# Kernel tuning notes

Hardware: AMD Instinct MI355X
Metric: run time of the kernel (lower is better)

Reference implementation:

```python
import jax, jax.numpy as jnp
import numpy as np

B, N, C, T = 16, 96, 4, 256
H, DT, DP, P, TOUT = 128, 16, 128, 4, 64
DIN = H + DT
LEAK = 0.1


def setup_inputs():
    key = jax.random.key(0)
    ks = jax.random.split(key, 16)
    rn = lambda k, shp, s: jax.random.normal(k, shp, dtype=jnp.float32) * s
    return {
        'X_in': jax.random.normal(ks[0], (B, N, C, T), dtype=jnp.float32),
        'phases': jax.random.randint(ks[1], (B,), 0, P),
        'gru_Wih': rn(ks[2], (N, 3 * H, C), 0.1),
        'gru_Whh': rn(ks[3], (N, 3 * H, H), 0.08),
        'gru_bih': jnp.zeros((N, 3 * H), jnp.float32),
        'gru_bhh': jnp.zeros((N, 3 * H), jnp.float32),
        'ln_g': jnp.ones((H,), jnp.float32),
        'ln_b': jnp.zeros((H,), jnp.float32),
        'tpos_w': rn(ks[4], (DT, 1), 0.5),
        'tpos_b': jnp.zeros((DT,), jnp.float32),
        'S': rn(ks[5], (P, N, N), 0.1),
        'G': rn(ks[6], (P, N), 0.1),
        'W_self': rn(ks[7], (DP, DIN), 0.05),
        'W_neigh': rn(ks[8], (DP, DIN), 0.05),
        'sn_u': jax.random.normal(ks[9], (DP,), dtype=jnp.float32),
        'k_w': rn(ks[10], (DP, DP), 0.05),
        'v_w': rn(ks[11], (DP, DP), 0.05),
        'cell_Wih': rn(ks[12], (3 * DP, DP + C), 0.05),
        'cell_Whh': rn(ks[13], (3 * DP, DP), 0.05),
        'cell_bih': jnp.zeros((3 * DP,), jnp.float32),
        'cell_bhh': jnp.zeros((3 * DP,), jnp.float32),
        'read_w': rn(ks[14], (C, DP), 0.05),
        'read_b': jnp.zeros((C,), jnp.float32),
        'log_tau': jnp.asarray(np.log(1.0 / np.sqrt(DP)), dtype=jnp.float32),
    }


def _encode(X, Wih, Whh, bih, bhh, g, b):
    # Per-region GRU (distinct weights per node), torch gate order r,z,n.
    xs = jnp.moveaxis(X, -1, 0)  # [T,B,N,C]
    h0 = jnp.zeros((B, N, H), X.dtype)
    def step(h, xt):
        gi = jnp.einsum('bnc,ngc->bng', xt, Wih) + bih
        gh = jnp.einsum('bnh,ngh->bng', h, Whh) + bhh
        ir, iz, inn = jnp.split(gi, 3, axis=-1)
        hr, hz, hn = jnp.split(gh, 3, axis=-1)
        r = jax.nn.sigmoid(ir + hr)
        z = jax.nn.sigmoid(iz + hz)
        n = jnp.tanh(inn + r * hn)
        hnew = (1.0 - z) * n + z * h
        return hnew, hnew
    _, ys = jax.lax.scan(step, h0, xs)  # [T,B,N,H]
    mu = ys.mean(-1, keepdims=True)
    var = ys.var(-1, keepdims=True)
    ys = (ys - mu) * jax.lax.rsqrt(var + 1e-5) * g + b
    return jnp.moveaxis(ys, 0, 2)  # [B,N,T,H]


def _phase_adj(S, G, phases):
    I = jnp.eye(N, dtype=S.dtype)
    S0 = S * (1.0 - I)
    denom = jnp.clip(jnp.abs(S0).sum(-1, keepdims=True), 1e-6, None)
    An = S0 / denom
    gg = jax.nn.softplus(G) + 1e-6
    gg = gg * (N / jnp.clip(gg.sum(-1, keepdims=True), 1e-6, None))
    return An[phases] * gg[phases][..., None]  # [B,N,N]


def _spectral_normalize(W, u):
    v = W.T @ u
    v = v / (jnp.linalg.norm(v) + 1e-12)
    u2 = W @ v
    u2 = u2 / (jnp.linalg.norm(u2) + 1e-12)
    u2 = jax.lax.stop_gradient(u2)
    v = jax.lax.stop_gradient(v)
    sigma = u2 @ (W @ v)
    return W / sigma


def _head(Z, A, k_w, v_w, cWih, cWhh, cbih, cbhh, rw, rb, log_tau):
    BN = B * N
    M = Z.reshape(BN, T, DP)
    K = M @ k_w.T
    V = M @ v_w.T
    h0 = M[:, -1, :]
    y0 = jnp.zeros((BN, C), Z.dtype)
    scale = jnp.exp(log_tau)
    def step(carry, _):
        h, y = carry
        yb = y.reshape(B, N, C)
        yb = yb + 0.3 * jnp.einsum('bij,bjc->bic', A, yb)
        y = yb.reshape(BN, C)
        scores = jnp.einsum('mtd,md->mt', K, h) * scale
        alpha = jax.nn.softmax(scores, axis=-1)
        ctx = jnp.einsum('mt,mtd->md', alpha, V)
        inp = jnp.concatenate([ctx, y], axis=-1)
        gi = inp @ cWih.T + cbih
        gh = h @ cWhh.T + cbhh
        ir, iz, inn = jnp.split(gi, 3, axis=-1)
        hr, hz, hn = jnp.split(gh, 3, axis=-1)
        r = jax.nn.sigmoid(ir + hr)
        z = jax.nn.sigmoid(iz + hz)
        n = jnp.tanh(inn + r * hn)
        h = (1.0 - z) * n + z * h
        y_t = h @ rw.T + rb + y
        return (h, y_t), y_t
    _, ys = jax.lax.scan(step, (h0, y0), None, length=TOUT)  # [TOUT,BN,C]
    return jnp.transpose(ys, (1, 2, 0)).reshape(B, N, C, TOUT)


def _forward(X_in, phases, gru_Wih, gru_Whh, gru_bih, gru_bhh, ln_g, ln_b,
             tpos_w, tpos_b, S, G, W_self, W_neigh, sn_u, k_w, v_w,
             cell_Wih, cell_Whh, cell_bih, cell_bhh, read_w, read_b, log_tau):
    Henc = _encode(X_in, gru_Wih, gru_Whh, gru_bih, gru_bhh, ln_g, ln_b)  # [B,N,T,H]
    t = jnp.linspace(0.0, 1.0, T).astype(jnp.float32).reshape(T, 1)
    u = jnp.tanh(t @ tpos_w.T + tpos_b)  # [T,DT]
    u = jnp.broadcast_to(u[None, None], (B, N, T, DT))
    Hc = jnp.concatenate([Henc, u], axis=-1)  # [B,N,T,DIN]
    A = _phase_adj(S, G, phases)
    Wsn = _spectral_normalize(W_neigh, sn_u)
    Hs = Hc @ W_self.T
    Hn = Hc @ Wsn.T
    Zn = jnp.einsum('bij,bjtd->bitd', A, Hn)
    Zpre = Hs + Zn
    Z = jnp.where(Zpre >= 0, Zpre, LEAK * Zpre)
    Y_delta = _head(Z, A, k_w, v_w, cell_Wih, cell_Whh, cell_bih, cell_bhh,
                    read_w, read_b, log_tau)
    x_last = X_in[..., -1]  # [B,N,C]
    Y_hat = x_last[..., None] + Y_delta
    return Y_hat, Y_hat[..., 0:1]


def reference(X_in, phases, gru_Wih, gru_Whh, gru_bih, gru_bhh, ln_g, ln_b,
              tpos_w, tpos_b, S, G, W_self, W_neigh, sn_u, k_w, v_w,
              cell_Wih, cell_Whh, cell_bih, cell_bhh, read_w, read_b, log_tau):
    return _forward(X_in, phases, gru_Wih, gru_Whh, gru_bih, gru_bhh, ln_g, ln_b,
                    tpos_w, tpos_b, S, G, W_self, W_neigh, sn_u, k_w, v_w,
                    cell_Wih, cell_Whh, cell_bih, cell_bhh, read_w, read_b, log_tau)
```

## Files before the change

kernel.cpp:

```cpp
#include <hip/hip_runtime.h>
#include <stdint.h>

typedef unsigned int u32;
typedef unsigned short u16;
typedef unsigned char u8;
typedef __attribute__((ext_vector_type(8))) short s8v;
typedef __attribute__((ext_vector_type(8))) __bf16 bf16x8;
typedef __attribute__((ext_vector_type(4))) float f32x4;

#define OFF_HENC 0ull
#define OFF_M    100663296ull
#define OFF_MI8  201326592ull
#define OFF_MSCL 251658240ull
#define OFF_APF  253231104ull
#define OFF_APB  253378560ull
#define OFF_WNF  253452288ull
#define OFF_WSF  253493248ull
#define OFF_KWF  253534208ull
#define OFF_VWF  253566976ull
#define OFF_WIHF 253599744ull
#define OFF_WHHF 253698048ull
#define OFF_CWY  253796352ull
#define OFF_UPAD 253802496ull
#define OFF_SCAL 253818880ull
#define OFF_HH   253819136ull
#define OFF_Y    254605568ull

__device__ __forceinline__ u16 f2bf(float f) {
  u32 u = __float_as_uint(f);
  u32 r = u + 0x7fffu + ((u >> 16) & 1u);
  return (u16)(r >> 16);
}
__device__ __forceinline__ float bf2f(u16 h) { return __uint_as_float(((u32)h) << 16); }
__device__ __forceinline__ float blo(u32 u) { return __uint_as_float(u << 16); }
__device__ __forceinline__ float bhi(u32 u) { return __uint_as_float(u & 0xffff0000u); }
__device__ __forceinline__ float sigm(float x) { return 1.f / (1.f + __expf(-x)); }
__device__ __forceinline__ float tanh_f(float x) {
  float a = fminf(fabsf(x), 15.f);
  float e = __expf(2.f * a);
  float t = (e - 1.f) / (e + 1.f);
  return copysignf(t, x);
}
__device__ __forceinline__ f32x4 MFMA(s8v a, s8v b, f32x4 c) {
  return __builtin_amdgcn_mfma_f32_16x16x32_bf16(
      __builtin_bit_cast(bf16x8, a), __builtin_bit_cast(bf16x8, b), c, 0, 0, 0);
}
__device__ __forceinline__ float ub0(u32 x) { return (float)(x & 0xffu); }
__device__ __forceinline__ float ub1(u32 x) { return (float)((x >> 8) & 0xffu); }
__device__ __forceinline__ float ub2(u32 x) { return (float)((x >> 16) & 0xffu); }
__device__ __forceinline__ float ub3(u32 x) { return (float)((x >> 24) & 0xffu); }

#define LGKM_BARRIER()                                        \
  do {                                                        \
    asm volatile("s_waitcnt lgkmcnt(0)" ::: "memory");        \
    __builtin_amdgcn_s_barrier();                             \
  } while (0)

__global__ void k0a(const float* __restrict__ S, const float* __restrict__ G,
                    const float* __restrict__ Wn, const float* __restrict__ snu,
                    const float* __restrict__ logtau, const float* __restrict__ tpw,
                    const float* __restrict__ tpb, const float* __restrict__ cWih,
                    float* __restrict__ Apf, u16* __restrict__ Apb,
                    float* __restrict__ scal, u16* __restrict__ upad,
                    float* __restrict__ cWy) {
  int tid = threadIdx.x;
  int blk = blockIdx.x;
  if (blk < 4) {
    int p = blk;
    __shared__ float gg[96];
    __shared__ float gfac;
    if (tid < 96) {
      float x = G[p * 96 + tid];
      float sp = fmaxf(x, 0.f) + log1pf(__expf(-fabsf(x)));
      gg[tid] = sp + 1e-6f;
    }
    __syncthreads();
    if (tid == 0) {
      float s = 0;
      for (int i = 0; i < 96; ++i) s += gg[i];
      gfac = 96.f / fmaxf(s, 1e-6f);
    }
    __syncthreads();
    if (tid < 96) {
      int i = tid;
      const float* srow = S + ((size_t)p * 96 + i) * 96;
      float den = 0;
      for (int j = 0; j < 96; ++j) { float v = (j == i) ? 0.f : srow[j]; den += fabsf(v); }
      den = fmaxf(den, 1e-6f);
      float sc = gg[i] * gfac / den;
      for (int j = 0; j < 96; ++j) {
        float v = (j == i) ? 0.f : srow[j];
        float a = v * sc;
        Apf[((size_t)p * 96 + i) * 96 + j] = a;
        Apb[((size_t)p * 96 + i) * 96 + j] = f2bf(a);
      }
    }
  } else if (blk == 4) {
    __shared__ float sv[144];
    __shared__ float su[128];
    __shared__ float snorm;
    if (tid < 144) {
      float a = 0;
      for (int d = 0; d < 128; ++d) a += Wn[d * 144 + tid] * snu[d];
      sv[tid] = a;
    }
    __syncthreads();
    if (tid == 0) {
      float s = 0;
      for (int j = 0; j < 144; ++j) s += sv[j] * sv[j];
      snorm = sqrtf(s) + 1e-12f;
    }
    __syncthreads();
    if (tid < 144) sv[tid] = sv[tid] / snorm;
    __syncthreads();
    if (tid < 128) {
      float a = 0;
      for (int j = 0; j < 144; ++j) a += Wn[tid * 144 + j] * sv[j];
      su[tid] = a;
    }
    __syncthreads();
    if (tid == 0) {
      float ss = 0;
      for (int d = 0; d < 128; ++d) ss += su[d] * su[d];
      float nu = sqrtf(ss);
      float sigma = ss / (nu + 1e-12f);
      scal[0] = 1.f / sigma;
      scal[1] = __expf(logtau[0]);
    }
  } else {
    for (int idx = tid; idx < 256 * 32; idx += 256) {
      int t = idx >> 5, kk = idx & 31;
      float v = 0.f;
      if (kk < 16) v = tanh_f((float)t * (1.f / 255.f) * tpw[kk] + tpb[kk]);
      upad[idx] = f2bf(v);
    }
    for (int idx = tid; idx < 1536; idx += 256)
      cWy[idx] = cWih[(idx >> 2) * 132 + 128 + (idx & 3)];
  }
}

__global__ void k0b(const float* __restrict__ Wn, const float* __restrict__ Ws,
                    const float* __restrict__ kw, const float* __restrict__ vw,
                    const float* __restrict__ cWih, const float* __restrict__ cWhh,
                    const float* __restrict__ scal,
                    u16* __restrict__ WnF, u16* __restrict__ WsF,
                    u16* __restrict__ kwF, u16* __restrict__ vwF,
                    u16* __restrict__ wiF, u16* __restrict__ whF) {
  int idx = blockIdx.x * 256 + threadIdx.x;
  int lane, j, ctkq, ct, kq, col, k;
  if (idx < 20480) {
    ctkq = idx >> 9; lane = (idx >> 3) & 63; j = idx & 7;
    ct = ctkq / 5; kq = ctkq % 5;
    col = ct * 16 + (lane & 15); k = kq * 32 + ((lane >> 4) << 3) + j;
    float v = (k < 144) ? Wn[col * 144 + k] * scal[0] : 0.f;
    WnF[idx] = f2bf(v);
    return;
  }
  idx -= 20480;
  if (idx < 20480) {
    ctkq = idx >> 9; lane = (idx >> 3) & 63; j = idx & 7;
    ct = ctkq / 5; kq = ctkq % 5;
    col = ct * 16 + (lane & 15); k = kq * 32 + ((lane >> 4) << 3) + j;
    float v = (k < 144) ? Ws[col * 144 + k] : 0.f;
    WsF[idx] = f2bf(v);
    return;
  }
  idx -= 20480;
  if (idx < 16384) {
    ctkq = idx >> 9; lane = (idx >> 3) & 63; j = idx & 7;
    ct = ctkq >> 2; kq = ctkq & 3;
    col = ct * 16 + (lane & 15); k = kq * 32 + ((lane >> 4) << 3) + j;
    kwF[idx] = f2bf(kw[k * 128 + col]);
    return;
  }
  idx -= 16384;
  if (idx < 16384) {
    ctkq = idx >> 9; lane = (idx >> 3) & 63; j = idx & 7;
    ct = ctkq >> 2; kq = ctkq & 3;
    col = ct * 16 + (lane & 15); k = kq * 32 + ((lane >> 4) << 3) + j;
    vwF[idx] = f2bf(vw[col * 128 + k]);
    return;
  }
  idx -= 16384;
  if (idx < 49152) {
    ctkq = idx >> 9; lane = (idx >> 3) & 63; j = idx & 7;
    ct = ctkq >> 2; kq = ctkq & 3;
    col = ct * 16 + (lane & 15); k = kq * 32 + ((lane >> 4) << 3) + j;
    wiF[idx] = f2bf(cWih[col * 132 + k]);
    return;
  }
  idx -= 49152;
  if (idx < 49152) {
    ctkq = idx >> 9; lane = (idx >> 3) & 63; j = idx & 7;
    ct = ctkq >> 2; kq = ctkq & 3;
    col = ct * 16 + (lane & 15); k = kq * 32 + ((lane >> 4) << 3) + j;
    whF[idx] = f2bf(cWhh[col * 128 + k]);
  }
}

__launch_bounds__(512)
__global__ void k1_encode(const float* __restrict__ X, const float* __restrict__ Wih,
                          const float* __restrict__ Whh, const float* __restrict__ bih,
                          const float* __restrict__ bhh, u16* __restrict__ Henc) {
  const int n = blockIdx.x;
  const int lane = threadIdx.x & 63, w = threadIdx.x >> 6;
  const int colt = lane & 15, grp = lane >> 4;
  __shared__ __align__(16) float Xl[16][256][4];
  __shared__ __align__(16) u16 hb[2][16][136];

  for (int idx = threadIdx.x; idx < 16 * 1024; idx += 512) {
    int b = idx >> 10, rem = idx & 1023, c = rem >> 8, t = rem & 255;
    Xl[b][t][c] = X[(((size_t)b * 96 + n) * 4 + c) * 256 + t];
  }
  for (int idx = threadIdx.x; idx < 2 * 16 * 136; idx += 512) (&hb[0][0][0])[idx] = 0;

  s8v bfr[3][4];
#pragma unroll
  for (int g = 0; g < 3; ++g) {
    int col = g * 128 + w * 16 + colt;
    const float* wr = Whh + ((size_t)n * 384 + col) * 128;
#pragma unroll
    for (int kq = 0; kq < 4; ++kq) {
      int k0 = kq * 32 + grp * 8;
      float4 f0 = *(const float4*)(wr + k0);
      float4 f1 = *(const float4*)(wr + k0 + 4);
      union { s8v v; u16 s[8]; } tmp;
      tmp.s[0] = f2bf(f0.x); tmp.s[1] = f2bf(f0.y); tmp.s[2] = f2bf(f0.z); tmp.s[3] = f2bf(f0.w);
      tmp.s[4] = f2bf(f1.x); tmp.s[5] = f2bf(f1.y); tmp.s[6] = f2bf(f1.z); tmp.s[7] = f2bf(f1.w);
      bfr[g][kq] = tmp.v;
    }
  }
  float wihr[3][4], bi[3], bh[3];
#pragma unroll
  for (int g = 0; g < 3; ++g) {
    int col = g * 128 + w * 16 + colt;
    float4 wv = *(const float4*)(Wih + ((size_t)n * 384 + col) * 4);
    wihr[g][0] = wv.x; wihr[g][1] = wv.y; wihr[g][2] = wv.z; wihr[g][3] = wv.w;
    bi[g] = bih[n * 384 + col];
    bh[g] = bhh[n * 384 + col];
  }
  float h_reg[4] = {0.f, 0.f, 0.f, 0.f};
  __syncthreads();

  int cur = 0;
  for (int t = 0; t < 256; ++t) {
    s8v a[4];
#pragma unroll
    for (int kq = 0; kq < 4; ++kq)
      a[kq] = *(const s8v*)(const void*)&hb[cur][colt][kq * 32 + grp * 8];
    f32x4 acc0 = {0.f, 0.f, 0.f, 0.f}, acc1 = acc0, acc2 = acc0;
#pragma unroll
    for (int kq = 0; kq < 4; ++kq) {
      acc0 = MFMA(a[kq], bfr[0][kq], acc0);
      acc1 = MFMA(a[kq], bfr[1][kq], acc1);
      acc2 = MFMA(a[kq], bfr[2][kq], acc2);
    }
#pragma unroll
    for (int r = 0; r < 4; ++r) {
      int b = grp * 4 + r;
      float4 x4 = *(const float4*)&Xl[b][t][0];
      float gir = bi[0] + x4.x * wihr[0][0] + x4.y * wihr[0][1] + x4.z * wihr[0][2] + x4.w * wihr[0][3];
      float giz = bi[1] + x4.x * wihr[1][0] + x4.y * wihr[1][1] + x4.z * wihr[1][2] + x4.w * wihr[1][3];
      float gin = bi[2] + x4.x * wihr[2][0] + x4.y * wihr[2][1] + x4.z * wihr[2][2] + x4.w * wihr[2][3];
      float rr = sigm(gir + acc0[r] + bh[0]);
      float zz = sigm(giz + acc1[r] + bh[1]);
      float nn = tanh_f(gin + rr * (acc2[r] + bh[2]));
      float hv = (1.f - zz) * nn + zz * h_reg[r];
      h_reg[r] = hv;
      u16 hvb = f2bf(hv);
      Henc[(((size_t)b * 96 + n) * 256 + t) * 128 + w * 16 + colt] = hvb;
      hb[cur ^ 1][b][w * 16 + colt] = hvb;
    }
    LGKM_BARRIER();
    cur ^= 1;
  }
}

__launch_bounds__(256, 2)
__global__ void k3_mix(const u16* __restrict__ Henc, const u16* __restrict__ upad,
                       const u16* __restrict__ Apb, const int* __restrict__ phases,
                       const float* __restrict__ lng, const float* __restrict__ lnb,
                       const s8v* __restrict__ WnF, const s8v* __restrict__ WsF,
                       u16* __restrict__ M, float* __restrict__ hh) {
  const int b = blockIdx.x >> 8, t = blockIdx.x & 255;
  const int p = phases[b];
  const int lane = threadIdx.x & 63, w = threadIdx.x >> 6;
  const int colt = lane & 15, grp = lane >> 4;
  __shared__ __align__(16) u16 Hc[96][168];
  __shared__ __align__(16) u16 HnT[128][104];
  __shared__ float lnG[128], lnB[128];

  const u16* src = Henc + ((size_t)b * 96 * 256 + t) * 128;
  for (int u = threadIdx.x; u < 96 * 16; u += 256) {
    int j = u >> 4, ch = u & 15;
    *(uint4*)&Hc[j][ch * 8] = *(const uint4*)(src + (size_t)j * 256 * 128 + ch * 8);
  }
  for (int u = threadIdx.x; u < 96 * 16; u += 256) {
    int j = u >> 4, ch = u & 15;
    *(u32*)&Hc[j][128 + ch * 2] = *(const u32*)(upad + t * 32 + ch * 2);
  }
  if (threadIdx.x < 128) {
    lnG[threadIdx.x] = lng[threadIdx.x];
    lnB[threadIdx.x] = lnb[threadIdx.x];
  }
  __syncthreads();
  if (threadIdx.x < 96) {
    int j = threadIdx.x;
    float s = 0.f, q = 0.f;
#pragma unroll 4
    for (int d = 0; d < 128; ++d) {
      float v = bf2f(Hc[j][d]);
      s += v; q += v * v;
    }
    float mu = s * (1.f / 128.f);
    float var = q * (1.f / 128.f) - mu * mu;
    float rs = rsqrtf(var + 1e-5f);
#pragma unroll 4
    for (int d = 0; d < 128; ++d) {
      float v = bf2f(Hc[j][d]);
      Hc[j][d] = f2bf((v - mu) * rs * lnG[d] + lnB[d]);
    }
  }
  __syncthreads();
  for (int jj = 0; jj < 12; ++jj) {
    int job = w * 12 + jj;
    int jt = job >> 3, ct = job & 7;
    f32x4 acc = {0.f, 0.f, 0.f, 0.f};
#pragma unroll
    for (int kq = 0; kq < 5; ++kq) {
      s8v a = *(const s8v*)(const void*)&Hc[jt * 16 + colt][kq * 32 + grp * 8];
      acc = MFMA(a, WnF[(ct * 5 + kq) * 64 + lane], acc);
    }
    int d = ct * 16 + colt, j0 = jt * 16 + grp * 4;
    u32 w0 = ((u32)f2bf(acc[1]) << 16) | f2bf(acc[0]);
    u32 w1 = ((u32)f2bf(acc[3]) << 16) | f2bf(acc[2]);
    *(u32*)&HnT[d][j0] = w0;
    *(u32*)&HnT[d][j0 + 2] = w1;
  }
  __syncthreads();
  for (int jj = 0; jj < 12; ++jj) {
    int job = w * 12 + jj;
    int it = job >> 3, ct = job & 7;
    f32x4 accZ = {0.f, 0.f, 0.f, 0.f}, accS = accZ;
#pragma unroll
    for (int kq = 0; kq < 3; ++kq) {
      s8v a = *(const s8v*)(const void*)(Apb + ((size_t)p * 96 + it * 16 + colt) * 96 + kq * 32 + grp * 8);
      s8v bb = *(const s8v*)(const void*)&HnT[ct * 16 + colt][kq * 32 + grp * 8];
      accZ = MFMA(a, bb, accZ);
    }
#pragma unroll
    for (int kq = 0; kq < 5; ++kq) {
      s8v a = *(const s8v*)(const void*)&Hc[it * 16 + colt][kq * 32 + grp * 8];
      accS = MFMA(a, WsF[(ct * 5 + kq) * 64 + lane], accS);
    }
    int d = ct * 16 + colt;
#pragma unroll
    for (int r = 0; r < 4; ++r) {
      int i = it * 16 + grp * 4 + r;
      float z = accS[r] + accZ[r];
      z = z >= 0.f ? z : 0.1f * z;
      M[(((size_t)b * 96 + i) * 256 + t) * 128 + d] = f2bf(z);
      if (t == 255) hh[((size_t)b * 96 + i) * 128 + d] = z;
    }
  }
}

__launch_bounds__(256)
__global__ void k3b(const u16* __restrict__ Mbf, u8* __restrict__ Mi8,
                    float* __restrict__ Mscl) {
  const size_t m = blockIdx.x;
  const int t = threadIdx.x;
  const u16* src = Mbf + (m * 256 + t) * 128;
  float vals[128];
  float mx = 0.f;
#pragma unroll 8
  for (int d = 0; d < 128; ++d) {
    float f = bf2f(src[d]);
    vals[d] = f;
    mx = fmaxf(mx, fabsf(f));
  }
  float scale = mx * (1.f / 127.f);
  float inv = (mx > 0.f) ? (127.f / mx) : 0.f;
  u32* dst = (u32*)(Mi8 + (m * 256 + t) * 128);
#pragma unroll 8
  for (int dw = 0; dw < 32; ++dw) {
    u32 packed = 0;
#pragma unroll
    for (int j = 0; j < 4; ++j) {
      int q = (int)rintf(vals[dw * 4 + j] * inv) + 128;
      packed |= ((u32)(q & 0xff)) << (8 * j);
    }
    dst[dw] = packed;
  }
  Mscl[m * 256 + t] = scale;
}

__launch_bounds__(512)
__global__ void k4_step(int k, const u8* __restrict__ Mi8, const float* __restrict__ Mscl,
                        float* __restrict__ hh,
                        const float* __restrict__ yin, float* __restrict__ yout,
                        const float* __restrict__ Apf, const int* __restrict__ phases,
                        const float* __restrict__ scal,
                        const s8v* __restrict__ kwF, const s8v* __restrict__ vwF,
                        const s8v* __restrict__ wiF, const s8v* __restrict__ whF,
                        const float* __restrict__ cWy, const float* __restrict__ cbih,
                        const float* __restrict__ cbhh, const float* __restrict__ rw,
                        const float* __restrict__ rb, const float* __restrict__ X,
                        float* __restrict__ out) {
  const int bl = blockIdx.x;
  const int b = bl >> 4, n0 = (bl & 15) * 6, m0 = b * 96 + n0;
  const int lane = threadIdx.x & 63, w = threadIdx.x >> 6;
  const int colt = lane & 15, grp = lane >> 4;
  __shared__ float hfl[6][128];
  __shared__ __align__(16) u16 hb[16][136];
  __shared__ __align__(16) u16 qb[6][128];
  __shared__ __align__(16) u16 sb[16][136];
  __shared__ __align__(16) u16 cxb[16][136];
  __shared__ __align__(16) u32 maccb[6][16][64];
  __shared__ float mmd[6][16][4];
  __shared__ float sclL[6][256];
  __shared__ float gi_l[6][392];
  __shared__ float gh_l[6][392];
  __shared__ float ypl[6][4];
  const float scale = scal[1];

  for (int idx = threadIdx.x; idx < 2048; idx += 512) {
    int i = idx >> 7, d = idx & 127;
    float hv = 0.f;
    if (i < 6) {
      hv = hh[(size_t)(m0 + i) * 128 + d];
      hfl[i][d] = hv;
    } else {
      sb[i][d] = 0;
      cxb[i][d] = 0;
    }
    hb[i][d] = f2bf(hv);
  }
  for (int idx = threadIdx.x; idx < 1536; idx += 512) {
    int mi = idx >> 8, t = idx & 255;
    sclL[mi][t] = Mscl[(size_t)(m0 + mi) * 256 + t];
  }
  if (w < 6) {
    int i = w, ni = n0 + w;
    const float* arow = Apf + ((size_t)phases[b] * 96 + ni) * 96;
    float acc[4] = {0.f, 0.f, 0.f, 0.f};
    for (int j = lane; j < 96; j += 64) {
      float av = arow[j];
      const float* yr = yin + ((size_t)b * 96 + j) * 4;
      acc[0] += av * yr[0]; acc[1] += av * yr[1];
      acc[2] += av * yr[2]; acc[3] += av * yr[3];
    }
#pragma unroll
    for (int mm = 1; mm < 64; mm <<= 1) {
#pragma unroll
      for (int c = 0; c < 4; ++c) acc[c] += __shfl_xor(acc[c], mm);
    }
    if (lane < 4) ypl[i][lane] = yin[((size_t)b * 96 + ni) * 4 + lane] + 0.3f * acc[lane];
  }
  __syncthreads();

  {
    int ct = w;
    f32x4 acc = {0.f, 0.f, 0.f, 0.f};
#pragma unroll
    for (int kq = 0; kq < 4; ++kq) {
      s8v a = *(const s8v*)(const void*)&hb[colt][kq * 32 + grp * 8];
      acc = MFMA(a, kwF[(ct * 4 + kq) * 64 + lane], acc);
    }
#pragma unroll
    for (int r = 0; r < 4; ++r) {
      int i = grp * 4 + r;
      if (i < 6) qb[i][ct * 16 + colt] = f2bf(acc[r] * scale);
    }
  }
  __syncthreads();

#pragma unroll 1
  for (int uu = 0; uu < 3; ++uu) {
    int u = w + uu * 8;
    int mi = u >> 2, qq = u & 3;
    float qf[8];
    const u32* qsrc = (const u32*)&qb[mi][colt * 8];
#pragma unroll
    for (int x = 0; x < 4; ++x) { u32 v = qsrc[x]; qf[2 * x] = blo(v); qf[2 * x + 1] = bhi(v); }
    float qs = qf[0] + qf[1] + qf[2] + qf[3] + qf[4] + qf[5] + qf[6] + qf[7];
    qs += __shfl_xor(qs, 1); qs += __shfl_xor(qs, 2);
    qs += __shfl_xor(qs, 4); qs += __shfl_xor(qs, 8);
    const u8* mp = Mi8 + ((size_t)(m0 + mi) * 256 + qq * 64 + grp) * 128 + colt * 8;
    uint2 mv[16];
#pragma unroll
    for (int it = 0; it < 16; ++it) mv[it] = *(const uint2*)(mp + (size_t)it * 512);
    float scl[16];
#pragma unroll
    for (int it = 0; it < 16; ++it) scl[it] = sclL[mi][qq * 64 + it * 4 + grp];
    float p[16];
#pragma unroll
    for (int it = 0; it < 16; ++it) {
      uint2 v = mv[it];
      float pp = qf[0] * ub0(v.x) + qf[1] * ub1(v.x) + qf[2] * ub2(v.x) + qf[3] * ub3(v.x)
               + qf[4] * ub0(v.y) + qf[5] * ub1(v.y) + qf[6] * ub2(v.y) + qf[7] * ub3(v.y);
      pp += __shfl_xor(pp, 1); pp += __shfl_xor(pp, 2);
      pp += __shfl_xor(pp, 4); pp += __shfl_xor(pp, 8);
      p[it] = scl[it] * (pp - 128.f * qs);
    }
    float mx = p[0];
#pragma unroll
    for (int it = 1; it < 16; ++it) mx = fmaxf(mx, p[it]);
    float den = 0.f, gs = 0.f;
    float acc[8] = {0.f, 0.f, 0.f, 0.f, 0.f, 0.f, 0.f, 0.f};
#pragma unroll
    for (int it = 0; it < 16; ++it) {
      float wgt = __expf(p[it] - mx);
      den += wgt;
      float g = wgt * scl[it];
      gs += g;
      uint2 v = mv[it];
      acc[0] += g * ub0(v.x); acc[1] += g * ub1(v.x);
      acc[2] += g * ub2(v.x); acc[3] += g * ub3(v.x);
      acc[4] += g * ub0(v.y); acc[5] += g * ub1(v.y);
      acc[6] += g * ub2(v.y); acc[7] += g * ub3(v.y);
    }
    int su = qq * 4 + grp;
    u32* dst = &maccb[mi][su][colt * 4];
#pragma unroll
    for (int x = 0; x < 4; ++x)
      dst[x] = ((u32)f2bf(acc[2 * x + 1]) << 16) | f2bf(acc[2 * x]);
    if (colt == 0) { mmd[mi][su][0] = mx; mmd[mi][su][1] = den; mmd[mi][su][2] = gs; }
  }
  __syncthreads();

  if (w < 6) {
    int i = w;
    float MX = -3.0e38f;
#pragma unroll
    for (int uy = 0; uy < 16; ++uy) MX = fmaxf(MX, mmd[i][uy][0]);
    float DEN = 0.f, GS = 0.f, s0 = 0.f, s1 = 0.f;
    int c0 = lane * 2;
#pragma unroll
    for (int uy = 0; uy < 16; ++uy) {
      float fac = __expf(mmd[i][uy][0] - MX);
      DEN += fac * mmd[i][uy][1];
      GS += fac * mmd[i][uy][2];
      u32 pv = maccb[i][uy][lane];
      s0 += fac * blo(pv);
      s1 += fac * bhi(pv);
    }
    float rden = 1.f / DEN;
    float corr = 128.f * GS;
    *(u32*)&sb[i][c0] = ((u32)f2bf((s1 - corr) * rden) << 16) | f2bf((s0 - corr) * rden);
  }
  __syncthreads();

  {
    int ct = w;
    f32x4 acc = {0.f, 0.f, 0.f, 0.f};
#pragma unroll
    for (int kq = 0; kq < 4; ++kq) {
      s8v a = *(const s8v*)(const void*)&sb[colt][kq * 32 + grp * 8];
      acc = MFMA(a, vwF[(ct * 4 + kq) * 64 + lane], acc);
    }
#pragma unroll
    for (int r = 0; r < 4; ++r) {
      int i = grp * 4 + r;
      if (i < 6) cxb[i][ct * 16 + colt] = f2bf(acc[r]);
    }
  }
  __syncthreads();

  for (int jj = 0; jj < 6; ++jj) {
    int job = w * 6 + jj;
    int gsel = (job >= 24) ? 1 : 0;
    int ct = job - gsel * 24;
    const u16(*asrc)[136] = gsel ? hb : cxb;
    const s8v* wf = gsel ? whF : wiF;
    f32x4 acc = {0.f, 0.f, 0.f, 0.f};
#pragma unroll
    for (int kq = 0; kq < 4; ++kq) {
      s8v a = *(const s8v*)(const void*)&asrc[colt][kq * 32 + grp * 8];
      acc = MFMA(a, wf[(ct * 4 + kq) * 64 + lane], acc);
    }
    float* dst = gsel ? &gh_l[0][0] : &gi_l[0][0];
#pragma unroll
    for (int r = 0; r < 4; ++r) {
      int i = grp * 4 + r;
      if (i < 6) dst[i * 392 + ct * 16 + colt] = acc[r];
    }
  }
  __syncthreads();

  if (w < 6) {
    int i = w, m = m0 + i;
    float yp0 = ypl[i][0], yp1 = ypl[i][1], yp2 = ypl[i][2], yp3 = ypl[i][3];
    float hn2[2];
#pragma unroll
    for (int q = 0; q < 2; ++q) {
      int d = lane + q * 64;
      float gir = gi_l[i][d] + cbih[d];
      float giz = gi_l[i][d + 128] + cbih[d + 128];
      float gin = gi_l[i][d + 256] + cbih[d + 256];
      const float* wy0 = cWy + (size_t)d * 4;
      const float* wy1 = cWy + (size_t)(d + 128) * 4;
      const float* wy2 = cWy + (size_t)(d + 256) * 4;
      gir += yp0 * wy0[0] + yp1 * wy0[1] + yp2 * wy0[2] + yp3 * wy0[3];
      giz += yp0 * wy1[0] + yp1 * wy1[1] + yp2 * wy1[2] + yp3 * wy1[3];
      gin += yp0 * wy2[0] + yp1 * wy2[1] + yp2 * wy2[2] + yp3 * wy2[3];
      float ghr = gh_l[i][d] + cbhh[d];
      float ghz = gh_l[i][d + 128] + cbhh[d + 128];
      float ghn = gh_l[i][d + 256] + cbhh[d + 256];
      float rr = sigm(gir + ghr);
      float zz = sigm(giz + ghz);
      float nn = tanh_f(gin + rr * ghn);
      float hv = (1.f - zz) * nn + zz * hfl[i][d];
      hh[(size_t)m * 128 + d] = hv;
      hn2[q] = hv;
    }
    float p0 = hn2[0] * rw[0 * 128 + lane] + hn2[1] * rw[0 * 128 + lane + 64];
    float p1 = hn2[0] * rw[1 * 128 + lane] + hn2[1] * rw[1 * 128 + lane + 64];
    float p2 = hn2[0] * rw[2 * 128 + lane] + hn2[1] * rw[2 * 128 + lane + 64];
    float p3 = hn2[0] * rw[3 * 128 + lane] + hn2[1] * rw[3 * 128 + lane + 64];
#pragma unroll
    for (int mm = 1; mm < 64; mm <<= 1) {
      p0 += __shfl_xor(p0, mm); p1 += __shfl_xor(p1, mm);
      p2 += __shfl_xor(p2, mm); p3 += __shfl_xor(p3, mm);
    }
    if (lane < 4) {
      int c = lane;
      float pv = (c == 0) ? p0 : (c == 1) ? p1 : (c == 2) ? p2 : p3;
      float ypc = (c == 0) ? yp0 : (c == 1) ? yp1 : (c == 2) ? yp2 : yp3;
      float yv = pv + rb[c] + ypc;
      yout[(size_t)m * 4 + c] = yv;
      float xl = X[((size_t)m * 4 + c) * 256 + 255];
      float Yh = xl + yv;
      out[((size_t)m * 4 + c) * 64 + k] = Yh;
      if (k == 0) out[393216 + (size_t)m * 4 + c] = Yh;
    }
  }
}

extern "C" void kernel_launch(void* const* d_in, const int* in_sizes, int n_in,
                              void* d_out, int out_size, void* d_ws, size_t ws_size,
                              hipStream_t stream) {
  const float* X      = (const float*)d_in[0];
  const int*   phases = (const int*)d_in[1];
  const float* Wih    = (const float*)d_in[2];
  const float* Whh    = (const float*)d_in[3];
  const float* bih    = (const float*)d_in[4];
  const float* bhh    = (const float*)d_in[5];
  const float* lng    = (const float*)d_in[6];
  const float* lnb    = (const float*)d_in[7];
  const float* tpw    = (const float*)d_in[8];
  const float* tpb    = (const float*)d_in[9];
  const float* S      = (const float*)d_in[10];
  const float* G      = (const float*)d_in[11];
  const float* Wself  = (const float*)d_in[12];
  const float* Wneigh = (const float*)d_in[13];
  const float* snu    = (const float*)d_in[14];
  const float* kw     = (const float*)d_in[15];
  const float* vw     = (const float*)d_in[16];
  const float* cWih   = (const float*)d_in[17];
  const float* cWhh   = (const float*)d_in[18];
  const float* cbih   = (const float*)d_in[19];
  const float* cbhh   = (const float*)d_in[20];
  const float* rw     = (const float*)d_in[21];
  const float* rb     = (const float*)d_in[22];
  const float* ltau   = (const float*)d_in[23];

  char* ws = (char*)d_ws;
  u16*   Henc = (u16*)(ws + OFF_HENC);
  u16*   Mb   = (u16*)(ws + OFF_M);
  u8*    Mi8  = (u8*)(ws + OFF_MI8);
  float* Mscl = (float*)(ws + OFF_MSCL);
  float* Apf  = (float*)(ws + OFF_APF);
  u16*   Apb  = (u16*)(ws + OFF_APB);
  u16*   WnF  = (u16*)(ws + OFF_WNF);
  u16*   WsF  = (u16*)(ws + OFF_WSF);
  u16*   kwF  = (u16*)(ws + OFF_KWF);
  u16*   vwF  = (u16*)(ws + OFF_VWF);
  u16*   wiF  = (u16*)(ws + OFF_WIHF);
  u16*   whF  = (u16*)(ws + OFF_WHHF);
  float* cWy  = (float*)(ws + OFF_CWY);
  u16*   upad = (u16*)(ws + OFF_UPAD);
  float* scal = (float*)(ws + OFF_SCAL);
  float* hh   = (float*)(ws + OFF_HH);

  hipMemsetAsync(ws + OFF_Y, 0, 49152, stream);
  hipLaunchKernelGGL(k0a, dim3(6), dim3(256), 0, stream,
                     S, G, Wneigh, snu, ltau, tpw, tpb, cWih, Apf, Apb, scal, upad, cWy);
  hipLaunchKernelGGL(k0b, dim3(672), dim3(256), 0, stream,
                     Wneigh, Wself, kw, vw, cWih, cWhh, scal, WnF, WsF, kwF, vwF, wiF, whF);
  hipLaunchKernelGGL(k1_encode, dim3(96), dim3(512), 0, stream,
                     X, Wih, Whh, bih, bhh, Henc);
  hipLaunchKernelGGL(k3_mix, dim3(4096), dim3(256), 0, stream,
                     Henc, upad, Apb, phases, lng, lnb,
                     (const s8v*)WnF, (const s8v*)WsF, Mb, hh);
  hipLaunchKernelGGL(k3b, dim3(1536), dim3(256), 0, stream, Mb, Mi8, Mscl);
  for (int k = 0; k < 64; ++k) {
    const float* yi = (const float*)(ws + OFF_Y + (size_t)(k & 1) * 24576);
    float*       yo = (float*)(ws + OFF_Y + (size_t)((k + 1) & 1) * 24576);
    hipLaunchKernelGGL(k4_step, dim3(256), dim3(512), 0, stream,
                       k, Mi8, Mscl, hh, yi, yo, Apf, phases, scal,
                       (const s8v*)kwF, (const s8v*)vwF, (const s8v*)wiF, (const s8v*)whF,
                       cWy, cbih, cbhh, rw, rb, X, (float*)d_out);
  }
}
```

Measured before the change: 2.076 ms.

## Fuse 64 decode-step launches into one persistent kernel with per-batch barriers

Replaces the 64 per-step k4_step launches with a single persistent kernel that loops over the steps internally. Blocks of the same batch sync through a global atomic counter/generation barrier, and y values are exchanged with agent-scope atomic loads and stores. The hidden state stays in shared memory, and small weights (biases, cWy, read weights, adjacency rows, last-step X values) are loaded into LDS once. This removes launch overhead and the per-step reloads, but it depends on all 256 blocks being co-resident to avoid deadlock and adds spin-wait cost.

```diff
diff --git a/kernel.cpp b/kernel.cpp
--- a/kernel.cpp
+++ b/kernel.cpp
@@ -25,6 +25,7 @@
 #define OFF_SCAL 253818880ull
 #define OFF_HH   253819136ull
 #define OFF_Y    254605568ull
+#define OFF_BAR  254654720ull
 
 __device__ __forceinline__ u16 f2bf(float f) {
   u32 u = __float_as_uint(f);
@@ -395,22 +396,41 @@
   Mscl[m * 256 + t] = scale;
 }
 
+__device__ __forceinline__ void group_barrier(int* cnt, int* gen) {
+  __syncthreads();
+  if (threadIdx.x == 0) {
+    int g = __hip_atomic_load(gen, __ATOMIC_RELAXED, __HIP_MEMORY_SCOPE_AGENT);
+    int v = __hip_atomic_fetch_add(cnt, 1, __ATOMIC_ACQ_REL, __HIP_MEMORY_SCOPE_AGENT);
+    if (v == 15) {
+      __hip_atomic_store(cnt, 0, __ATOMIC_RELAXED, __HIP_MEMORY_SCOPE_AGENT);
+      __hip_atomic_fetch_add(gen, 1, __ATOMIC_ACQ_REL, __HIP_MEMORY_SCOPE_AGENT);
+    } else {
+      while (__hip_atomic_load(gen, __ATOMIC_ACQUIRE, __HIP_MEMORY_SCOPE_AGENT) == g)
+        __builtin_amdgcn_s_sleep(2);
+    }
+  }
+  __syncthreads();
+}
+
 __launch_bounds__(512)
-__global__ void k4_step(int k, const u8* __restrict__ Mi8, const float* __restrict__ Mscl,
-                        float* __restrict__ hh,
-                        const float* __restrict__ yin, float* __restrict__ yout,
-                        const float* __restrict__ Apf, const int* __restrict__ phases,
-                        const float* __restrict__ scal,
-                        const s8v* __restrict__ kwF, const s8v* __restrict__ vwF,
-                        const s8v* __restrict__ wiF, const s8v* __restrict__ whF,
-                        const float* __restrict__ cWy, const float* __restrict__ cbih,
-                        const float* __restrict__ cbhh, const float* __restrict__ rw,
-                        const float* __restrict__ rb, const float* __restrict__ X,
-                        float* __restrict__ out) {
+__global__ void k4p(const u8* __restrict__ Mi8, const float* __restrict__ Mscl,
+                    const float* __restrict__ hh,
+                    float* __restrict__ ybuf, int* __restrict__ bar,
+                    const float* __restrict__ Apf, const int* __restrict__ phases,
+                    const float* __restrict__ scal,
+                    const s8v* __restrict__ kwF, const s8v* __restrict__ vwF,
+                    const s8v* __restrict__ wiF, const s8v* __restrict__ whF,
+                    const float* __restrict__ cWy, const float* __restrict__ cbih,
+                    const float* __restrict__ cbhh, const float* __restrict__ rw,
+                    const float* __restrict__ rb, const float* __restrict__ X,
+                    float* __restrict__ out) {
   const int bl = blockIdx.x;
   const int b = bl >> 4, n0 = (bl & 15) * 6, m0 = b * 96 + n0;
   const int lane = threadIdx.x & 63, w = threadIdx.x >> 6;
   const int colt = lane & 15, grp = lane >> 4;
+  int* cnt = bar + b;
+  int* gen = bar + 16 + b;
+
   __shared__ float hfl[6][128];
   __shared__ __align__(16) u16 hb[16][136];
   __shared__ __align__(16) u16 qb[6][128];
@@ -422,6 +442,14 @@
   __shared__ float gi_l[6][392];
   __shared__ float gh_l[6][392];
   __shared__ float ypl[6][4];
+  __shared__ float Arows[6][96];
+  __shared__ float cbl_i[384], cbl_h[384];
+  __shared__ float cWyl[384][4];
+  __shared__ float rwl[4][128];
+  __shared__ float rbl[4];
+  __shared__ float xlast[6][4];
+
+  const int p = phases[b];
   const float scale = scal[1];
 
   for (int idx = threadIdx.x; idx < 2048; idx += 512) {
@@ -440,200 +468,233 @@
     int mi = idx >> 8, t = idx & 255;
     sclL[mi][t] = Mscl[(size_t)(m0 + mi) * 256 + t];
   }
-  if (w < 6) {
-    int i = w, ni = n0 + w;
-    const float* arow = Apf + ((size_t)phases[b] * 96 + ni) * 96;
-    float acc[4] = {0.f, 0.f, 0.f, 0.f};
-    for (int j = lane; j < 96; j += 64) {
-      float av = arow[j];
-      const float* yr = yin + ((size_t)b * 96 + j) * 4;
-      acc[0] += av * yr[0]; acc[1] += av * yr[1];
-      acc[2] += av * yr[2]; acc[3] += av * yr[3];
-    }
-#pragma unroll
-    for (int mm = 1; mm < 64; mm <<= 1) {
-#pragma unroll
-      for (int c = 0; c < 4; ++c) acc[c] += __shfl_xor(acc[c], mm);
-    }
-    if (lane < 4) ypl[i][lane] = yin[((size_t)b * 96 + ni) * 4 + lane] + 0.3f * acc[lane];
-  }
+  for (int idx = threadIdx.x; idx < 576; idx += 512) {
+    int i = idx / 96, j = idx % 96;
+    Arows[i][j] = Apf[((size_t)p * 96 + (n0 + i)) * 96 + j];
+  }
+  if (threadIdx.x < 384) {
+    cbl_i[threadIdx.x] = cbih[threadIdx.x];
+    cbl_h[threadIdx.x] = cbhh[threadIdx.x];
+  }
+  for (int idx = threadIdx.x; idx < 1536; idx += 512)
+    (&cWyl[0][0])[idx] = cWy[idx];
+  if (threadIdx.x < 512) (&rwl[0][0])[threadIdx.x] = rw[threadIdx.x];
+  if (threadIdx.x < 4) rbl[threadIdx.x] = rb[threadIdx.x];
+  if (threadIdx.x < 24)
+    xlast[threadIdx.x >> 2][threadIdx.x & 3] =
+        X[((size_t)(m0 + (threadIdx.x >> 2)) * 4 + (threadIdx.x & 3)) * 256 + 255];
   __syncthreads();
 
-  {
-    int ct = w;
-    f32x4 acc = {0.f, 0.f, 0.f, 0.f};
-#pragma unroll
-    for (int kq = 0; kq < 4; ++kq) {
-      s8v a = *(const s8v*)(const void*)&hb[colt][kq * 32 + grp * 8];
-      acc = MFMA(a, kwF[(ct * 4 + kq) * 64 + lane], acc);
-    }
-#pragma unroll
-    for (int r = 0; r < 4; ++r) {
-      int i = grp * 4 + r;
-      if (i < 6) qb[i][ct * 16 + colt] = f2bf(acc[r] * scale);
-    }
-  }
-  __syncthreads();
-
 #pragma unroll 1
-  for (int uu = 0; uu < 3; ++uu) {
-    int u = w + uu * 8;
-    int mi = u >> 2, qq = u & 3;
-    float qf[8];
-    const u32* qsrc = (const u32*)&qb[mi][colt * 8];
-#pragma unroll
-    for (int x = 0; x < 4; ++x) { u32 v = qsrc[x]; qf[2 * x] = blo(v); qf[2 * x + 1] = bhi(v); }
-    float qs = qf[0] + qf[1] + qf[2] + qf[3] + qf[4] + qf[5] + qf[6] + qf[7];
-    qs += __shfl_xor(qs, 1); qs += __shfl_xor(qs, 2);
-    qs += __shfl_xor(qs, 4); qs += __shfl_xor(qs, 8);
-    const u8* mp = Mi8 + ((size_t)(m0 + mi) * 256 + qq * 64 + grp) * 128 + colt * 8;
-    uint2 mv[16];
-#pragma unroll
-    for (int it = 0; it < 16; ++it) mv[it] = *(const uint2*)(mp + (size_t)it * 512);
-    float scl[16];
-#pragma unroll
-    for (int it = 0; it < 16; ++it) scl[it] = sclL[mi][qq * 64 + it * 4 + grp];
-    float p[16];
-#pragma unroll
-    for (int it = 0; it < 16; ++it) {
-      uint2 v = mv[it];
-      float pp = qf[0] * ub0(v.x) + qf[1] * ub1(v.x) + qf[2] * ub2(v.x) + qf[3] * ub3(v.x)
-               + qf[4] * ub0(v.y) + qf[5] * ub1(v.y) + qf[6] * ub2(v.y) + qf[7] * ub3(v.y);
-      pp += __shfl_xor(pp, 1); pp += __shfl_xor(pp, 2);
-      pp += __shfl_xor(pp, 4); pp += __shfl_xor(pp, 8);
-      p[it] = scl[it] * (pp - 128.f * qs);
-    }
-    float mx = p[0];
-#pragma unroll
-    for (int it = 1; it < 16; ++it) mx = fmaxf(mx, p[it]);
-    float den = 0.f, gs = 0.f;
-    float acc[8] = {0.f, 0.f, 0.f, 0.f, 0.f, 0.f, 0.f, 0.f};
-#pragma unroll
-    for (int it = 0; it < 16; ++it) {
-      float wgt = __expf(p[it] - mx);
-      den += wgt;
-      float g = wgt * scl[it];
-      gs += g;
-      uint2 v = mv[it];
-      acc[0] += g * ub0(v.x); acc[1] += g * ub1(v.x);
-      acc[2] += g * ub2(v.x); acc[3] += g * ub3(v.x);
-      acc[4] += g * ub0(v.y); acc[5] += g * ub1(v.y);
-      acc[6] += g * ub2(v.y); acc[7] += g * ub3(v.y);
-    }
-    int su = qq * 4 + grp;
-    u32* dst = &maccb[mi][su][colt * 4];
-#pragma unroll
-    for (int x = 0; x < 4; ++x)
-      dst[x] = ((u32)f2bf(acc[2 * x + 1]) << 16) | f2bf(acc[2 * x]);
-    if (colt == 0) { mmd[mi][su][0] = mx; mmd[mi][su][1] = den; mmd[mi][su][2] = gs; }
-  }
-  __syncthreads();
-
-  if (w < 6) {
-    int i = w;
-    float MX = -3.0e38f;
-#pragma unroll
-    for (int uy = 0; uy < 16; ++uy) MX = fmaxf(MX, mmd[i][uy][0]);
-    float DEN = 0.f, GS = 0.f, s0 = 0.f, s1 = 0.f;
-    int c0 = lane * 2;
-#pragma unroll
-    for (int uy = 0; uy < 16; ++uy) {
-      float fac = __expf(mmd[i][uy][0] - MX);
-      DEN += fac * mmd[i][uy][1];
-      GS += fac * mmd[i][uy][2];
-      u32 pv = maccb[i][uy][lane];
-      s0 += fac * blo(pv);
-      s1 += fac * bhi(pv);
-    }
-    float rden = 1.f / DEN;
-    float corr = 128.f * GS;
-    *(u32*)&sb[i][c0] = ((u32)f2bf((s1 - corr) * rden) << 16) | f2bf((s0 - corr) * rden);
-  }
-  __syncthreads();
-
-  {
-    int ct = w;
-    f32x4 acc = {0.f, 0.f, 0.f, 0.f};
-#pragma unroll
-    for (int kq = 0; kq < 4; ++kq) {
-      s8v a = *(const s8v*)(const void*)&sb[colt][kq * 32 + grp * 8];
-      acc = MFMA(a, vwF[(ct * 4 + kq) * 64 + lane], acc);
-    }
-#pragma unroll
-    for (int r = 0; r < 4; ++r) {
-      int i = grp * 4 + r;
-      if (i < 6) cxb[i][ct * 16 + colt] = f2bf(acc[r]);
-    }
-  }
-  __syncthreads();
-
-  for (int jj = 0; jj < 6; ++jj) {
-    int job = w * 6 + jj;
-    int gsel = (job >= 24) ? 1 : 0;
-    int ct = job - gsel * 24;
-    const u16(*asrc)[136] = gsel ? hb : cxb;
-    const s8v* wf = gsel ? whF : wiF;
-    f32x4 acc = {0.f, 0.f, 0.f, 0.f};
-#pragma unroll
-    for (int kq = 0; kq < 4; ++kq) {
-      s8v a = *(const s8v*)(const void*)&asrc[colt][kq * 32 + grp * 8];
-      acc = MFMA(a, wf[(ct * 4 + kq) * 64 + lane], acc);
-    }
-    float* dst = gsel ? &gh_l[0][0] : &gi_l[0][0];
-#pragma unroll
-    for (int r = 0; r < 4; ++r) {
-      int i = grp * 4 + r;
-      if (i < 6) dst[i * 392 + ct * 16 + colt] = acc[r];
-    }
-  }
-  __syncthreads();
-
-  if (w < 6) {
-    int i = w, m = m0 + i;
-    float yp0 = ypl[i][0], yp1 = ypl[i][1], yp2 = ypl[i][2], yp3 = ypl[i][3];
-    float hn2[2];
-#pragma unroll
-    for (int q = 0; q < 2; ++q) {
-      int d = lane + q * 64;
-      float gir = gi_l[i][d] + cbih[d];
-      float giz = gi_l[i][d + 128] + cbih[d + 128];
-      float gin = gi_l[i][d + 256] + cbih[d + 256];
-      const float* wy0 = cWy + (size_t)d * 4;
-      const float* wy1 = cWy + (size_t)(d + 128) * 4;
-      const float* wy2 = cWy + (size_t)(d + 256) * 4;
-      gir += yp0 * wy0[0] + yp1 * wy0[1] + yp2 * wy0[2] + yp3 * wy0[3];
-      giz += yp0 * wy1[0] + yp1 * wy1[1] + yp2 * wy1[2] + yp3 * wy1[3];
-      gin += yp0 * wy2[0] + yp1 * wy2[1] + yp2 * wy2[2] + yp3 * wy2[3];
-      float ghr = gh_l[i][d] + cbhh[d];
-      float ghz = gh_l[i][d + 128] + cbhh[d + 128];
-      float ghn = gh_l[i][d + 256] + cbhh[d + 256];
-      float rr = sigm(gir + ghr);
-      float zz = sigm(giz + ghz);
-      float nn = tanh_f(gin + rr * ghn);
-      float hv = (1.f - zz) * nn + zz * hfl[i][d];
-      hh[(size_t)m * 128 + d] = hv;
-      hn2[q] = hv;
-    }
-    float p0 = hn2[0] * rw[0 * 128 + lane] + hn2[1] * rw[0 * 128 + lane + 64];
-    float p1 = hn2[0] * rw[1 * 128 + lane] + hn2[1] * rw[1 * 128 + lane + 64];
-    float p2 = hn2[0] * rw[2 * 128 + lane] + hn2[1] * rw[2 * 128 + lane + 64];
-    float p3 = hn2[0] * rw[3 * 128 + lane] + hn2[1] * rw[3 * 128 + lane + 64];
-#pragma unroll
-    for (int mm = 1; mm < 64; mm <<= 1) {
-      p0 += __shfl_xor(p0, mm); p1 += __shfl_xor(p1, mm);
-      p2 += __shfl_xor(p2, mm); p3 += __shfl_xor(p3, mm);
-    }
-    if (lane < 4) {
-      int c = lane;
-      float pv = (c == 0) ? p0 : (c == 1) ? p1 : (c == 2) ? p2 : p3;
-      float ypc = (c == 0) ? yp0 : (c == 1) ? yp1 : (c == 2) ? yp2 : yp3;
-      float yv = pv + rb[c] + ypc;
-      yout[(size_t)m * 4 + c] = yv;
-      float xl = X[((size_t)m * 4 + c) * 256 + 255];
-      float Yh = xl + yv;
-      out[((size_t)m * 4 + c) * 64 + k] = Yh;
-      if (k == 0) out[393216 + (size_t)m * 4 + c] = Yh;
-    }
+  for (int k = 0; k < 64; ++k) {
+    const float* yin = ybuf + (size_t)(k & 1) * 6144;
+    float* yout = ybuf + (size_t)((k + 1) & 1) * 6144;
+
+    if (w < 6) {
+      int i = w, ni = n0 + w;
+      float a0 = 0.f, a1 = 0.f, a2 = 0.f, a3 = 0.f;
+#pragma unroll 1
+      for (int j = lane; j < 96; j += 64) {
+        float av = Arows[i][j];
+        float* yr = (float*)(yin + ((size_t)b * 96 + j) * 4);
+        a0 += av * __hip_atomic_load(yr + 0, __ATOMIC_RELAXED, __HIP_MEMORY_SCOPE_AGENT);
+        a1 += av * __hip_atomic_load(yr + 1, __ATOMIC_RELAXED, __HIP_MEMORY_SCOPE_AGENT);
+        a2 += av * __hip_atomic_load(yr + 2, __ATOMIC_RELAXED, __HIP_MEMORY_SCOPE_AGENT);
+        a3 += av * __hip_atomic_load(yr + 3, __ATOMIC_RELAXED, __HIP_MEMORY_SCOPE_AGENT);
+      }
+#pragma unroll
+      for (int mm = 1; mm < 64; mm <<= 1) {
+        a0 += __shfl_xor(a0, mm); a1 += __shfl_xor(a1, mm);
+        a2 += __shfl_xor(a2, mm); a3 += __shfl_xor(a3, mm);
+      }
+      if (lane < 4) {
+        float av = (lane == 0) ? a0 : (lane == 1) ? a1 : (lane == 2) ? a2 : a3;
+        float yo = __hip_atomic_load((float*)(yin + ((size_t)b * 96 + ni) * 4 + lane),
+                                     __ATOMIC_RELAXED, __HIP_MEMORY_SCOPE_AGENT);
+        ypl[i][lane] = yo + 0.3f * av;
+      }
+    }
+
+    {
+      int ct = w;
+      f32x4 acc = {0.f, 0.f, 0.f, 0.f};
+#pragma unroll
+      for (int kq = 0; kq < 4; ++kq) {
+        s8v a = *(const s8v*)(const void*)&hb[colt][kq * 32 + grp * 8];
+        acc = MFMA(a, kwF[(ct * 4 + kq) * 64 + lane], acc);
+      }
+#pragma unroll
+      for (int r = 0; r < 4; ++r) {
+        int i = grp * 4 + r;
+        if (i < 6) qb[i][ct * 16 + colt] = f2bf(acc[r] * scale);
+      }
+    }
+    __syncthreads();
+
+#pragma unroll 1
+    for (int uu = 0; uu < 3; ++uu) {
+      int u = w + uu * 8;
+      int mi = u >> 2, qq = u & 3;
+      float qf[8];
+      const u32* qsrc = (const u32*)&qb[mi][colt * 8];
+#pragma unroll
+      for (int x = 0; x < 4; ++x) { u32 v = qsrc[x]; qf[2 * x] = blo(v); qf[2 * x + 1] = bhi(v); }
+      float qs = qf[0] + qf[1] + qf[2] + qf[3] + qf[4] + qf[5] + qf[6] + qf[7];
+      qs += __shfl_xor(qs, 1); qs += __shfl_xor(qs, 2);
+      qs += __shfl_xor(qs, 4); qs += __shfl_xor(qs, 8);
+      const u8* mp = Mi8 + ((size_t)(m0 + mi) * 256 + qq * 64 + grp) * 128 + colt * 8;
+      uint2 mv[16];
+#pragma unroll
+      for (int it = 0; it < 16; ++it) mv[it] = *(const uint2*)(mp + (size_t)it * 512);
+      float scl[16];
+#pragma unroll
+      for (int it = 0; it < 16; ++it) scl[it] = sclL[mi][qq * 64 + it * 4 + grp];
+      float pr[16];
+#pragma unroll
+      for (int it = 0; it < 16; ++it) {
+        uint2 v = mv[it];
+        float pp = qf[0] * ub0(v.x) + qf[1] * ub1(v.x) + qf[2] * ub2(v.x) + qf[3] * ub3(v.x)
+                 + qf[4] * ub0(v.y) + qf[5] * ub1(v.y) + qf[6] * ub2(v.y) + qf[7] * ub3(v.y);
+        pp += __shfl_xor(pp, 1); pp += __shfl_xor(pp, 2);
+        pp += __shfl_xor(pp, 4); pp += __shfl_xor(pp, 8);
+        pr[it] = scl[it] * (pp - 128.f * qs);
+      }
+      float mx = pr[0];
+#pragma unroll
+      for (int it = 1; it < 16; ++it) mx = fmaxf(mx, pr[it]);
+      float den = 0.f, gs = 0.f;
+      float acc[8] = {0.f, 0.f, 0.f, 0.f, 0.f, 0.f, 0.f, 0.f};
+#pragma unroll
+      for (int it = 0; it < 16; ++it) {
+        float wgt = __expf(pr[it] - mx);
+        den += wgt;
+        float g = wgt * scl[it];
+        gs += g;
+        uint2 v = mv[it];
+        acc[0] += g * ub0(v.x); acc[1] += g * ub1(v.x);
+        acc[2] += g * ub2(v.x); acc[3] += g * ub3(v.x);
+        acc[4] += g * ub0(v.y); acc[5] += g * ub1(v.y);
+        acc[6] += g * ub2(v.y); acc[7] += g * ub3(v.y);
+      }
+      int su = qq * 4 + grp;
+      u32* dst = &maccb[mi][su][colt * 4];
+#pragma unroll
+      for (int x = 0; x < 4; ++x)
+        dst[x] = ((u32)f2bf(acc[2 * x + 1]) << 16) | f2bf(acc[2 * x]);
+      if (colt == 0) { mmd[mi][su][0] = mx; mmd[mi][su][1] = den; mmd[mi][su][2] = gs; }
+    }
+    __syncthreads();
+
+    if (w < 6) {
+      int i = w;
+      float MX = -3.0e38f;
+#pragma unroll
+      for (int uy = 0; uy < 16; ++uy) MX = fmaxf(MX, mmd[i][uy][0]);
+      float DEN = 0.f, GS = 0.f, s0 = 0.f, s1 = 0.f;
+      int c0 = lane * 2;
+#pragma unroll
+      for (int uy = 0; uy < 16; ++uy) {
+        float fac = __expf(mmd[i][uy][0] - MX);
+        DEN += fac * mmd[i][uy][1];
+        GS += fac * mmd[i][uy][2];
+        u32 pv = maccb[i][uy][lane];
+        s0 += fac * blo(pv);
+        s1 += fac * bhi(pv);
+      }
+      float rden = 1.f / DEN;
+      float corr = 128.f * GS;
+      *(u32*)&sb[i][c0] = ((u32)f2bf((s1 - corr) * rden) << 16) | f2bf((s0 - corr) * rden);
+    }
+    __syncthreads();
+
+    {
+      int ct = w;
+      f32x4 acc = {0.f, 0.f, 0.f, 0.f};
+#pragma unroll
+      for (int kq = 0; kq < 4; ++kq) {
+        s8v a = *(const s8v*)(const void*)&sb[colt][kq * 32 + grp * 8];
+        acc = MFMA(a, vwF[(ct * 4 + kq) * 64 + lane], acc);
+      }
+#pragma unroll
+      for (int r = 0; r < 4; ++r) {
+        int i = grp * 4 + r;
+        if (i < 6) cxb[i][ct * 16 + colt] = f2bf(acc[r]);
+      }
+    }
+    __syncthreads();
+
+#pragma unroll 1
+    for (int jj = 0; jj < 6; ++jj) {
+      int job = w * 6 + jj;
+      int gsel = (job >= 24) ? 1 : 0;
+      int ct = job - gsel * 24;
+      const u16(*asrc)[136] = gsel ? hb : cxb;
+      const s8v* wf = gsel ? whF : wiF;
+      f32x4 acc = {0.f, 0.f, 0.f, 0.f};
+#pragma unroll
+      for (int kq = 0; kq < 4; ++kq) {
+        s8v a = *(const s8v*)(const void*)&asrc[colt][kq * 32 + grp * 8];
+        acc = MFMA(a, wf[(ct * 4 + kq) * 64 + lane], acc);
+      }
+      float* dst = gsel ? &gh_l[0][0] : &gi_l[0][0];
+#pragma unroll
+      for (int r = 0; r < 4; ++r) {
+        int i = grp * 4 + r;
+        if (i < 6) dst[i * 392 + ct * 16 + colt] = acc[r];
+      }
+    }
+    __syncthreads();
+
+    if (w < 6) {
+      int i = w, m = m0 + i;
+      float yp0 = ypl[i][0], yp1 = ypl[i][1], yp2 = ypl[i][2], yp3 = ypl[i][3];
+      float hn2[2];
+#pragma unroll
+      for (int q = 0; q < 2; ++q) {
+        int d = lane + q * 64;
+        float gir = gi_l[i][d] + cbl_i[d];
+        float giz = gi_l[i][d + 128] + cbl_i[d + 128];
+        float gin = gi_l[i][d + 256] + cbl_i[d + 256];
+        const float* wy0 = &cWyl[d][0];
+        const float* wy1 = &cWyl[d + 128][0];
+        const float* wy2 = &cWyl[d + 256][0];
+        gir += yp0 * wy0[0] + yp1 * wy0[1] + yp2 * wy0[2] + yp3 * wy0[3];
+        giz += yp0 * wy1[0] + yp1 * wy1[1] + yp2 * wy1[2] + yp3 * wy1[3];
+        gin += yp0 * wy2[0] + yp1 * wy2[1] + yp2 * wy2[2] + yp3 * wy2[3];
+        float ghr = gh_l[i][d] + cbl_h[d];
+        float ghz = gh_l[i][d + 128] + cbl_h[d + 128];
+        float ghn = gh_l[i][d + 256] + cbl_h[d + 256];
+        float rg = sigm(gir + ghr);
+        float zz = sigm(giz + ghz);
+        float nn = tanh_f(gin + rg * ghn);
+        float hv = (1.f - zz) * nn + zz * hfl[i][d];
+        hfl[i][d] = hv;
+        hb[i][d] = f2bf(hv);
+        hn2[q] = hv;
+      }
+      float p0 = hn2[0] * rwl[0][lane] + hn2[1] * rwl[0][(lane + 64) & 127];
+      float p1 = hn2[0] * rwl[1][lane] + hn2[1] * rwl[1][(lane + 64) & 127];
+      float p2 = hn2[0] * rwl[2][lane] + hn2[1] * rwl[2][(lane + 64) & 127];
+      float p3 = hn2[0] * rwl[3][lane] + hn2[1] * rwl[3][(lane + 64) & 127];
+#pragma unroll
+      for (int mm = 1; mm < 64; mm <<= 1) {
+        p0 += __shfl_xor(p0, mm); p1 += __shfl_xor(p1, mm);
+        p2 += __shfl_xor(p2, mm); p3 += __shfl_xor(p3, mm);
+      }
+      if (lane < 4) {
+        int c = lane;
+        float pvv = (c == 0) ? p0 : (c == 1) ? p1 : (c == 2) ? p2 : p3;
+        float ypc = (c == 0) ? yp0 : (c == 1) ? yp1 : (c == 2) ? yp2 : yp3;
+        float yv = pvv + rbl[c] + ypc;
+        __hip_atomic_store((float*)(yout + (size_t)m * 4 + c), yv,
+                           __ATOMIC_RELAXED, __HIP_MEMORY_SCOPE_AGENT);
+        float Yh = xlast[i][c] + yv;
+        out[((size_t)m * 4 + c) * 64 + k] = Yh;
+        if (k == 0) out[393216 + (size_t)m * 4 + c] = Yh;
+      }
+    }
+
+    if (k < 63) group_barrier(cnt, gen);
   }
 }
 
@@ -682,8 +743,10 @@
   u16*   upad = (u16*)(ws + OFF_UPAD);
   float* scal = (float*)(ws + OFF_SCAL);
   float* hh   = (float*)(ws + OFF_HH);
-
-  hipMemsetAsync(ws + OFF_Y, 0, 49152, stream);
+  float* ybuf = (float*)(ws + OFF_Y);
+  int*   bar  = (int*)(ws + OFF_BAR);
+
+  hipMemsetAsync(ws + OFF_Y, 0, 49152 + 128, stream);
   hipLaunchKernelGGL(k0a, dim3(6), dim3(256), 0, stream,
                      S, G, Wneigh, snu, ltau, tpw, tpb, cWih, Apf, Apb, scal, upad, cWy);
   hipLaunchKernelGGL(k0b, dim3(672), dim3(256), 0, stream,
@@ -694,12 +757,8 @@
                      Henc, upad, Apb, phases, lng, lnb,
                      (const s8v*)WnF, (const s8v*)WsF, Mb, hh);
   hipLaunchKernelGGL(k3b, dim3(1536), dim3(256), 0, stream, Mb, Mi8, Mscl);
-  for (int k = 0; k < 64; ++k) {
-    const float* yi = (const float*)(ws + OFF_Y + (size_t)(k & 1) * 24576);
-    float*       yo = (float*)(ws + OFF_Y + (size_t)((k + 1) & 1) * 24576);
-    hipLaunchKernelGGL(k4_step, dim3(256), dim3(512), 0, stream,
-                       k, Mi8, Mscl, hh, yi, yo, Apf, phases, scal,
-                       (const s8v*)kwF, (const s8v*)vwF, (const s8v*)wiF, (const s8v*)whF,
-                       cWy, cbih, cbhh, rw, rb, X, (float*)d_out);
-  }
-}
+  hipLaunchKernelGGL(k4p, dim3(256), dim3(512), 0, stream,
+                     Mi8, Mscl, hh, ybuf, bar, Apf, phases, scal,
+                     (const s8v*)kwF, (const s8v*)vwF, (const s8v*)wiF, (const s8v*)whF,
+                     cWy, cbih, cbhh, rw, rb, X, (float*)d_out);
+}
```

After: 3.563 ms. +71.6%, slower.
